# Optimization experiments

Hardware: AMD Instinct MI355X
Metric: run time of the kernel (lower is better)

## Reference

```python
import jax, jax.numpy as jnp
import numpy as np

PEP_LEN = 15
IN_CH = 512
OUT_CH = 512
BATCH = 8192


def setup_inputs() -> dict:
    key = jax.random.key(0)
    k_x, k_w = jax.random.split(key)
    peptide_x = jax.random.normal(k_x, (BATCH, PEP_LEN, IN_CH), dtype=jnp.float32)
    # truncated_normal_(std=0.02) init; plain normal*0.02 is fine for a numeric reference
    weight = jax.random.normal(k_w, (PEP_LEN, IN_CH, OUT_CH), dtype=jnp.float32) * 0.02
    bias = jnp.zeros((PEP_LEN, OUT_CH), dtype=jnp.float32)
    return {"peptide_x": peptide_x, "weight": weight, "bias": bias}


def reference(peptide_x, weight, bias) -> jnp.ndarray:
    # Original torch code does a full tensordot over all pep_len positions
    # ([B,P,P,O]) then gathers the diagonal. That is mathematically identical
    # to a per-position batched matmul, which we compute directly.
    out = jnp.einsum('bpi,pio->bpo', peptide_x, weight)  # [B, P, O]
    return out + bias  # bias broadcasts over batch
```

## Files before the change

kernel.cpp:

```cpp
#include <hip/hip_runtime.h>
#include <hip/hip_bf16.h>
#include <stdint.h>

#define BATCH 8192
#define PEP 15
#define INC 512
#define OUTC 512
#define XROW (PEP*INC)
#define WT_P_ELEMS (INC*OUTC)
#define NSTEPS 16

typedef float f32x4 __attribute__((ext_vector_type(4)));
typedef short s16x8 __attribute__((ext_vector_type(8)));
typedef unsigned int u32x4 __attribute__((ext_vector_type(4)));

__device__ __forceinline__ ushort f2b(float v) {
  uint u = __float_as_uint(v);
  u += 0x7fffu + ((u >> 16) & 1u);
  return (ushort)(u >> 16);
}

__device__ __forceinline__ uint cvtpk(float a, float b) {
  uint r;
  asm("v_cvt_pk_bf16_f32 %0, %1, %2" : "=v"(r) : "v"(a), "v"(b));
  return r;
}

__global__ __launch_bounds__(256) void wt_kernel(const float* __restrict__ w,
                                                 ushort* __restrict__ wt) {
  __shared__ float tile[32 * 133];
  const int t = threadIdx.x;
  const int bid = blockIdx.x;
  const int nchunk = bid & 3;
  const int ks     = (bid >> 2) & 15;
  const int p      = bid >> 6;

  const float* src = w + (size_t)p * WT_P_ELEMS + (size_t)(ks * 32) * OUTC + nchunk * 128;
  const int rk = t >> 5;
  const int rc = (t & 31) * 4;
#pragma unroll
  for (int i = 0; i < 4; ++i) {
    const int k = rk + i * 8;
    f32x4 v = *(const f32x4*)(src + (size_t)k * OUTC + rc);
    *(f32x4*)&tile[k * 133 + rc] = v;
  }
  __syncthreads();

  ushort* dst = wt + ((size_t)(p * 16 + ks) * 32 + nchunk * 8) * 512;
#pragma unroll
  for (int h = 0; h < 2; ++h) {
    const int f   = t + h * 256;
    const int n16 = f >> 6;
    const int l   = f & 63;
    const int fr  = l & 15;
    const int g   = l >> 4;
    s16x8 hv;
#pragma unroll
    for (int e = 0; e < 8; ++e)
      hv[e] = (short)f2b(tile[(g * 8 + e) * 133 + n16 * 16 + fr]);
    *(s16x8*)(dst + (size_t)n16 * 512 + l * 8) = hv;
  }
}

__global__ __launch_bounds__(512, 4) void gemm_kernel(const float* __restrict__ x,
                                                      const ushort* __restrict__ wt,
                                                      const float* __restrict__ bias,
                                                      float* __restrict__ out) {
  __shared__ __align__(16) char lds_raw[65536];
  auto Ash = (ushort (*)[8][64][8])lds_raw;
  auto Bsh = (ushort (*)[16][64][8])(lds_raw + 16384);

  const int t    = threadIdx.x;
  const int lane = t & 63;
  const int wid  = t >> 6;
  const int wm   = wid >> 2;
  const int wn   = wid & 3;
  const int fr   = lane & 15;
  const int g    = lane >> 4;

  const int bid  = blockIdx.x;
  const int xcd  = bid & 7;
  const int j    = bid >> 3;
  const int n2   = j & 1;
  const int pair = xcd * 120 + (j >> 1);
  const int mb   = pair & 63;
  const int p    = pair >> 6;
  const int m0   = mb * 128;

  const float* asrc = x + (size_t)(m0 + wid * 16 + fr) * XROW + p * INC + g * 8;
  const ushort* bsrc = wt + (size_t)p * WT_P_ELEMS
                     + (size_t)(n2 * 16 + wid * 2) * 512 + (size_t)lane * 8;

  f32x4 acc[4][4] = {};
  f32x4 pa0, pa1;

  auto cvt_store = [&](int buf) {
    u32x4 aw;
    aw[0] = cvtpk(pa0[0], pa0[1]); aw[1] = cvtpk(pa0[2], pa0[3]);
    aw[2] = cvtpk(pa1[0], pa1[1]); aw[3] = cvtpk(pa1[2], pa1[3]);
    *(u32x4*)&Ash[buf][wid][lane][0] = aw;
  };
  auto stageB = [&](int ks, int buf) {
#pragma unroll
    for (int q = 0; q < 2; ++q) {
      __builtin_amdgcn_global_load_lds(
          (const __attribute__((address_space(1))) void*)(bsrc + (size_t)ks * 16384 + q * 512),
          (__attribute__((address_space(3))) void*)(&Bsh[buf][wid * 2 + q][lane][0]),
          16, 0, 0);
    }
  };

  pa0 = *(const f32x4*)(asrc);
  pa1 = *(const f32x4*)(asrc + 4);
  cvt_store(0);
  __builtin_amdgcn_sched_barrier(0);
  pa0 = *(const f32x4*)(asrc + 32);
  pa1 = *(const f32x4*)(asrc + 36);
  __builtin_amdgcn_sched_barrier(0);
  stageB(0, 0);
  stageB(1, 1);
  __builtin_amdgcn_sched_barrier(0);
  asm volatile("s_waitcnt vmcnt(2)" ::: "memory");
  asm volatile("s_waitcnt lgkmcnt(0)" ::: "memory");
  __builtin_amdgcn_s_barrier();
  __builtin_amdgcn_sched_barrier(0);

#pragma unroll
  for (int ks = 0; ks < NSTEPS; ++ks) {
    const int cur  = ks & 1;
    const int curB = ks % 3;

    if (ks + 1 < NSTEPS) cvt_store((ks + 1) & 1);
    __builtin_amdgcn_sched_barrier(0);

    if (ks + 2 < NSTEPS) {
      pa0 = *(const f32x4*)(asrc + (ks + 2) * 32);
      pa1 = *(const f32x4*)(asrc + (ks + 2) * 32 + 4);
    }
    __builtin_amdgcn_sched_barrier(0);

    if (ks + 2 < NSTEPS) stageB(ks + 2, (ks + 2) % 3);
    __builtin_amdgcn_sched_barrier(0);

    s16x8 af[4], bf[4];
#pragma unroll
    for (int i = 0; i < 4; ++i)
      af[i] = *(const s16x8*)&Ash[cur][wm * 4 + i][lane][0];
#pragma unroll
    for (int nf = 0; nf < 4; ++nf)
      bf[nf] = *(const s16x8*)&Bsh[curB][wn * 4 + nf][lane][0];

    __builtin_amdgcn_s_setprio(1);
#pragma unroll
    for (int i = 0; i < 4; ++i)
#pragma unroll
      for (int nf = 0; nf < 4; ++nf)
        acc[i][nf] = __builtin_amdgcn_mfma_f32_16x16x32_bf16(af[i], bf[nf], acc[i][nf], 0, 0, 0);
    __builtin_amdgcn_s_setprio(0);
    __builtin_amdgcn_sched_barrier(0);

    if (ks <= 13)      asm volatile("s_waitcnt vmcnt(4)" ::: "memory");
    else if (ks == 14) asm volatile("s_waitcnt vmcnt(0)" ::: "memory");
    asm volatile("s_waitcnt lgkmcnt(0)" ::: "memory");
    __builtin_amdgcn_s_barrier();
    __builtin_amdgcn_sched_barrier(0);
  }

  const int n0q = wn * 64;
  float bv[4];
#pragma unroll
  for (int nf = 0; nf < 4; ++nf) bv[nf] = bias[p * OUTC + n2 * 256 + n0q + nf * 16 + fr];

  float* reg0 = (float*)lds_raw;
  float* reg1 = (float*)lds_raw + 16 * 260;
  float* myreg = wm ? reg1 : reg0;
  const float* obase = out + p * INC + n2 * 256 + lane * 4;

#pragma unroll
  for (int s = 0; s < 4; ++s) {
    __builtin_amdgcn_sched_barrier(0);
#pragma unroll
    for (int nf = 0; nf < 4; ++nf)
#pragma unroll
      for (int r = 0; r < 4; ++r)
        myreg[(g * 4 + r) * 260 + n0q + nf * 16 + fr] = acc[s][nf][r] + bv[nf];
    __builtin_amdgcn_sched_barrier(0);
    asm volatile("s_waitcnt lgkmcnt(0)" ::: "memory");
    __builtin_amdgcn_s_barrier();
    __builtin_amdgcn_sched_barrier(0);

#pragma unroll
    for (int pass = 0; pass < 4; ++pass) {
      const int row_id = pass * 8 + wid;
      const int rgn = row_id >> 4;
      const int rw  = row_id & 15;
      f32x4 v = *(const f32x4*)((rgn ? reg1 : reg0) + rw * 260 + lane * 4);
      __builtin_nontemporal_store(v,
          (f32x4*)((float*)obase + (size_t)(m0 + rgn * 64 + s * 16 + rw) * XROW));
    }
    __builtin_amdgcn_sched_barrier(0);
    asm volatile("s_waitcnt lgkmcnt(0)" ::: "memory");
    __builtin_amdgcn_s_barrier();
    __builtin_amdgcn_sched_barrier(0);
  }
}

__global__ void naive_kernel(const float* __restrict__ x, const float* __restrict__ w,
                             const float* __restrict__ bias, float* __restrict__ out) {
  size_t i = (size_t)blockIdx.x * 256 + threadIdx.x;
  if (i >= (size_t)BATCH * PEP * OUTC) return;
  int o  = (int)(i & (OUTC - 1));
  int pp = (int)((i >> 9) % PEP);
  size_t b = i / ((size_t)PEP * OUTC);
  const float* xr = x + b * XROW + pp * INC;
  const float* wc = w + (size_t)pp * INC * OUTC + o;
  float s = bias[pp * OUTC + o];
  for (int k = 0; k < INC; ++k) s += xr[k] * wc[(size_t)k * OUTC];
  out[i] = s;
}

extern "C" void kernel_launch(void* const* d_in, const int* in_sizes, int n_in,
                              void* d_out, int out_size, void* d_ws, size_t ws_size,
                              hipStream_t stream) {
  const float* x    = (const float*)d_in[0];
  const float* w    = (const float*)d_in[1];
  const float* bias = (const float*)d_in[2];
  float* out = (float*)d_out;

  const size_t wt_bytes = (size_t)PEP * INC * OUTC * sizeof(ushort);
  if (ws_size >= wt_bytes) {
    wt_kernel<<<960, 256, 0, stream>>>(w, (ushort*)d_ws);
    gemm_kernel<<<1920, 512, 0, stream>>>(x, (const ushort*)d_ws, bias, out);
  } else {
    size_t total = (size_t)BATCH * PEP * OUTC;
    naive_kernel<<<(int)((total + 255) / 256), 256, 0, stream>>>(x, w, bias, out);
  }
}
```

Measured before the change: 144.7 us.

## Widen gemm block to full output width with 1024 threads and double buffering

Each block now computes all 512 output channels for its 128-row tile, so each activation row chunk is loaded and converted to bf16 once instead of twice. The kernel uses 16 waves per block, a new per-thread A load mapping, and a larger LDS footprint for B. The B pipeline is reduced from a triple-buffered two-step prefetch to a double-buffered one-step prefetch, which may expose more memory latency.

```diff
diff --git a/kernel.cpp b/kernel.cpp
--- a/kernel.cpp
+++ b/kernel.cpp
@@ -12,7 +12,7 @@
 
 typedef float f32x4 __attribute__((ext_vector_type(4)));
 typedef short s16x8 __attribute__((ext_vector_type(8)));
-typedef unsigned int u32x4 __attribute__((ext_vector_type(4)));
+typedef unsigned int u32x2 __attribute__((ext_vector_type(2)));
 
 __device__ __forceinline__ ushort f2b(float v) {
   uint u = __float_as_uint(v);
@@ -62,43 +62,47 @@
   }
 }
 
-__global__ __launch_bounds__(512, 4) void gemm_kernel(const float* __restrict__ x,
-                                                      const ushort* __restrict__ wt,
-                                                      const float* __restrict__ bias,
-                                                      float* __restrict__ out) {
-  __shared__ __align__(16) char lds_raw[65536];
+__global__ __launch_bounds__(1024, 2) void gemm_kernel(const float* __restrict__ x,
+                                                       const ushort* __restrict__ wt,
+                                                       const float* __restrict__ bias,
+                                                       float* __restrict__ out) {
+  __shared__ __align__(16) char lds_raw[81920];
   auto Ash = (ushort (*)[8][64][8])lds_raw;
-  auto Bsh = (ushort (*)[16][64][8])(lds_raw + 16384);
+  auto Bsh = (ushort (*)[32][64][8])(lds_raw + 16384);
 
   const int t    = threadIdx.x;
   const int lane = t & 63;
   const int wid  = t >> 6;
-  const int wm   = wid >> 2;
-  const int wn   = wid & 3;
+  const int wm   = wid >> 3;
+  const int wn   = wid & 7;
   const int fr   = lane & 15;
   const int g    = lane >> 4;
 
   const int bid  = blockIdx.x;
   const int xcd  = bid & 7;
   const int j    = bid >> 3;
-  const int n2   = j & 1;
-  const int pair = xcd * 120 + (j >> 1);
+  const int pair = xcd * 120 + j;
   const int mb   = pair & 63;
   const int p    = pair >> 6;
   const int m0   = mb * 128;
 
-  const float* asrc = x + (size_t)(m0 + wid * 16 + fr) * XROW + p * INC + g * 8;
-  const ushort* bsrc = wt + (size_t)p * WT_P_ELEMS
-                     + (size_t)(n2 * 16 + wid * 2) * 512 + (size_t)lane * 8;
+  const int arow  = t >> 3;
+  const int kq    = t & 7;
+  const float* asrc = x + (size_t)(m0 + arow) * XROW + p * INC + kq * 4;
+  const int am16  = arow >> 4;
+  const int aslot = (arow & 15) + 16 * (kq >> 1);
+  const int aeoff = (kq & 1) * 4;
+
+  const ushort* bsrc = wt + (size_t)p * WT_P_ELEMS + (size_t)(wid * 2) * 512 + (size_t)lane * 8;
 
   f32x4 acc[4][4] = {};
-  f32x4 pa0, pa1;
+  f32x4 pa;
 
   auto cvt_store = [&](int buf) {
-    u32x4 aw;
-    aw[0] = cvtpk(pa0[0], pa0[1]); aw[1] = cvtpk(pa0[2], pa0[3]);
-    aw[2] = cvtpk(pa1[0], pa1[1]); aw[3] = cvtpk(pa1[2], pa1[3]);
-    *(u32x4*)&Ash[buf][wid][lane][0] = aw;
+    u32x2 aw;
+    aw[0] = cvtpk(pa[0], pa[1]);
+    aw[1] = cvtpk(pa[2], pa[3]);
+    *(u32x2*)&Ash[buf][am16][aslot][aeoff] = aw;
   };
   auto stageB = [&](int ks, int buf) {
 #pragma unroll
@@ -110,36 +114,30 @@
     }
   };
 
-  pa0 = *(const f32x4*)(asrc);
-  pa1 = *(const f32x4*)(asrc + 4);
+  pa = *(const f32x4*)(asrc);
   cvt_store(0);
   __builtin_amdgcn_sched_barrier(0);
-  pa0 = *(const f32x4*)(asrc + 32);
-  pa1 = *(const f32x4*)(asrc + 36);
-  __builtin_amdgcn_sched_barrier(0);
   stageB(0, 0);
-  stageB(1, 1);
-  __builtin_amdgcn_sched_barrier(0);
-  asm volatile("s_waitcnt vmcnt(2)" ::: "memory");
+  __builtin_amdgcn_sched_barrier(0);
+  pa = *(const f32x4*)(asrc + 32);
+  __builtin_amdgcn_sched_barrier(0);
+  asm volatile("s_waitcnt vmcnt(1)" ::: "memory");
   asm volatile("s_waitcnt lgkmcnt(0)" ::: "memory");
   __builtin_amdgcn_s_barrier();
   __builtin_amdgcn_sched_barrier(0);
 
 #pragma unroll
   for (int ks = 0; ks < NSTEPS; ++ks) {
-    const int cur  = ks & 1;
-    const int curB = ks % 3;
-
-    if (ks + 1 < NSTEPS) cvt_store((ks + 1) & 1);
-    __builtin_amdgcn_sched_barrier(0);
-
-    if (ks + 2 < NSTEPS) {
-      pa0 = *(const f32x4*)(asrc + (ks + 2) * 32);
-      pa1 = *(const f32x4*)(asrc + (ks + 2) * 32 + 4);
-    }
-    __builtin_amdgcn_sched_barrier(0);
-
-    if (ks + 2 < NSTEPS) stageB(ks + 2, (ks + 2) % 3);
+    const int cur = ks & 1;
+    const int nxt = cur ^ 1;
+
+    if (ks + 1 < NSTEPS) cvt_store(nxt);
+    __builtin_amdgcn_sched_barrier(0);
+
+    if (ks + 1 < NSTEPS) stageB(ks + 1, nxt);
+    __builtin_amdgcn_sched_barrier(0);
+
+    if (ks + 2 < NSTEPS) pa = *(const f32x4*)(asrc + (ks + 2) * 32);
     __builtin_amdgcn_sched_barrier(0);
 
     s16x8 af[4], bf[4];
@@ -148,7 +146,7 @@
       af[i] = *(const s16x8*)&Ash[cur][wm * 4 + i][lane][0];
 #pragma unroll
     for (int nf = 0; nf < 4; ++nf)
-      bf[nf] = *(const s16x8*)&Bsh[curB][wn * 4 + nf][lane][0];
+      bf[nf] = *(const s16x8*)&Bsh[cur][wn * 4 + nf][lane][0];
 
     __builtin_amdgcn_s_setprio(1);
 #pragma unroll
@@ -159,22 +157,20 @@
     __builtin_amdgcn_s_setprio(0);
     __builtin_amdgcn_sched_barrier(0);
 
-    if (ks <= 13)      asm volatile("s_waitcnt vmcnt(4)" ::: "memory");
+    if (ks <= 13)      asm volatile("s_waitcnt vmcnt(1)" ::: "memory");
     else if (ks == 14) asm volatile("s_waitcnt vmcnt(0)" ::: "memory");
     asm volatile("s_waitcnt lgkmcnt(0)" ::: "memory");
     __builtin_amdgcn_s_barrier();
     __builtin_amdgcn_sched_barrier(0);
   }
 
-  const int n0q = wn * 64;
   float bv[4];
 #pragma unroll
-  for (int nf = 0; nf < 4; ++nf) bv[nf] = bias[p * OUTC + n2 * 256 + n0q + nf * 16 + fr];
-
-  float* reg0 = (float*)lds_raw;
-  float* reg1 = (float*)lds_raw + 16 * 260;
-  float* myreg = wm ? reg1 : reg0;
-  const float* obase = out + p * INC + n2 * 256 + lane * 4;
+  for (int nf = 0; nf < 4; ++nf) bv[nf] = bias[p * OUTC + wn * 64 + nf * 16 + fr];
+
+  float* region0 = (float*)lds_raw;
+  float* region1 = region0 + 16 * 520;
+  float* myreg = wm ? region1 : region0;
 
 #pragma unroll
   for (int s = 0; s < 4; ++s) {
@@ -183,20 +179,23 @@
     for (int nf = 0; nf < 4; ++nf)
 #pragma unroll
       for (int r = 0; r < 4; ++r)
-        myreg[(g * 4 + r) * 260 + n0q + nf * 16 + fr] = acc[s][nf][r] + bv[nf];
+        myreg[(g * 4 + r) * 520 + wn * 64 + nf * 16 + fr] = acc[s][nf][r] + bv[nf];
     __builtin_amdgcn_sched_barrier(0);
     asm volatile("s_waitcnt lgkmcnt(0)" ::: "memory");
     __builtin_amdgcn_s_barrier();
     __builtin_amdgcn_sched_barrier(0);
 
 #pragma unroll
-    for (int pass = 0; pass < 4; ++pass) {
-      const int row_id = pass * 8 + wid;
+    for (int rr = 0; rr < 2; ++rr) {
+      const int row_id = wid * 2 + rr;
       const int rgn = row_id >> 4;
       const int rw  = row_id & 15;
-      f32x4 v = *(const f32x4*)((rgn ? reg1 : reg0) + rw * 260 + lane * 4);
-      __builtin_nontemporal_store(v,
-          (f32x4*)((float*)obase + (size_t)(m0 + rgn * 64 + s * 16 + rw) * XROW));
+      const float* srcrow = (rgn ? region1 : region0) + rw * 520;
+      float* dst = out + (size_t)(m0 + rgn * 64 + s * 16 + rw) * XROW + p * INC;
+      f32x4 v0 = *(const f32x4*)(srcrow + lane * 4);
+      f32x4 v1 = *(const f32x4*)(srcrow + 256 + lane * 4);
+      __builtin_nontemporal_store(v0, (f32x4*)(dst + lane * 4));
+      __builtin_nontemporal_store(v1, (f32x4*)(dst + 256 + lane * 4));
     }
     __builtin_amdgcn_sched_barrier(0);
     asm volatile("s_waitcnt lgkmcnt(0)" ::: "memory");
@@ -230,7 +229,7 @@
   const size_t wt_bytes = (size_t)PEP * INC * OUTC * sizeof(ushort);
   if (ws_size >= wt_bytes) {
     wt_kernel<<<960, 256, 0, stream>>>(w, (ushort*)d_ws);
-    gemm_kernel<<<1920, 512, 0, stream>>>(x, (const ushort*)d_ws, bias, out);
+    gemm_kernel<<<960, 1024, 0, stream>>>(x, (const ushort*)d_ws, bias, out);
   } else {
     size_t total = (size_t)BATCH * PEP * OUTC;
     naive_kernel<<<(int)((total + 255) / 256), 256, 0, stream>>>(x, w, bias, out);
```

Result: faster. 141.0 us (-2.6%).
